# Kernel tuning notes

Hardware: AMD Instinct MI355X
Metric: run time of the kernel (lower is better)

## Reference

```python
import jax, jax.numpy as jnp
import numpy as np


def setup_inputs() -> dict:
    key = jax.random.key(0)
    k1, k2 = jax.random.split(key)
    shape = (16, 3, 512, 512)
    y_true = jax.random.uniform(k1, shape, dtype=jnp.float32)
    y_pred = jax.random.uniform(k2, shape, dtype=jnp.float32)
    return {"y_true": y_true, "y_pred": y_pred}


def reference(y_true, y_pred):
    B, C, W, H = y_true.shape
    percent = 0.4
    index = int(W * H * percent - 1)  # quantile index into ascending sort
    # gray1 = mean over the 3 channels of y_pred  -> [B, W, H]
    gray = (y_pred[:, 0] + y_pred[:, 1] + y_pred[:, 2]) / 3.0
    # torch.topk(-gray, n)[0][:, index] == -(ascending-sorted gray)[index]
    thr = jnp.sort(gray.reshape(B, W * H), axis=1)[:, index]  # [B]
    mask = (gray <= thr[:, None, None]).astype(y_pred.dtype)  # [B, W, H]
    mask = mask[:, None, :, :]  # broadcast over 3 channels
    # mask*|y_pred - y_true| == |mask*y_pred - mask*y_true| since mask in {0,1}
    d = jnp.abs(y_pred - y_true)
    w = mask * 0.8 + (1.0 - mask) * 0.2
    return jnp.mean(w * d)
```

## Files before the change

### kernel.cpp

```cpp
#include <hip/hip_runtime.h>
#include <stdint.h>

#define NB 16
#define NPIX 262144
#define K_RANK 104856u
#define NB1 4096
#define CHUNK_CAP 256
#define CAP 65536
#define SENT 0xFFFFFFFFu
#define PAD(i) ((i) + ((i) >> 4))

__global__ void k_gray_hist(const float* __restrict__ yp, unsigned* __restrict__ hist1,
                            unsigned* __restrict__ zr, int zcount) {
    __shared__ unsigned h[NB1];
    const int tid = threadIdx.x;
    const int gtid = blockIdx.x * 256 + tid;
    if (gtid < zcount) zr[gtid] = 0;
    for (int i = tid; i < NB1; i += 256) h[i] = 0;
    __syncthreads();

    const int blk   = blockIdx.x;
    const int b     = blk >> 8;
    const int chunk = blk & 255;
    const long base = (long)b * 3 * NPIX;
    const int  o    = (chunk * 256 + tid) * 4;

    const float4 c0 = *(const float4*)(yp + base + o);
    const float4 c1 = *(const float4*)(yp + base + NPIX + o);
    const float4 c2 = *(const float4*)(yp + base + 2 * NPIX + o);

    float g0 = (c0.x + c1.x + c2.x) / 3.0f;
    float g1 = (c0.y + c1.y + c2.y) / 3.0f;
    float g2 = (c0.z + c1.z + c2.z) / 3.0f;
    float g3 = (c0.w + c1.w + c2.w) / 3.0f;

    atomicAdd(&h[__float_as_uint(g0) >> 20], 1u);
    atomicAdd(&h[__float_as_uint(g1) >> 20], 1u);
    atomicAdd(&h[__float_as_uint(g2) >> 20], 1u);
    atomicAdd(&h[__float_as_uint(g3) >> 20], 1u);
    __syncthreads();

    unsigned* gh = hist1 + b * NB1;
    for (int i = tid; i < NB1; i += 256) {
        unsigned v = h[i];
        if (v) atomicAdd(&gh[i], v);
    }
}

__global__ void k_scan1(const unsigned* __restrict__ hist1,
                        unsigned* __restrict__ rank1, unsigned* __restrict__ bin1) {
    __shared__ unsigned sh[NB1 + (NB1 >> 4)];
    __shared__ unsigned wave_sums[4];
    const int b   = blockIdx.x;
    const int tid = threadIdx.x;
    const unsigned* hb = hist1 + b * NB1;

    for (int i = tid; i < NB1; i += 256) sh[PAD(i)] = hb[i];
    __syncthreads();

    unsigned sum = 0;
    #pragma unroll
    for (int j = 0; j < 16; ++j) sum += sh[tid * 17 + j];
    unsigned inc = sum;
    for (int off = 1; off < 64; off <<= 1) {
        unsigned v = __shfl_up(inc, off);
        if ((tid & 63) >= off) inc += v;
    }
    if ((tid & 63) == 63) wave_sums[tid >> 6] = inc;
    __syncthreads();
    unsigned woff = 0;
    for (int w = 0; w < (tid >> 6); ++w) woff += wave_sums[w];
    const unsigned excl = woff + inc - sum;

    const unsigned r = K_RANK;
    if (r >= excl && r < excl + sum) {
        unsigned cum = excl;
        unsigned d   = (unsigned)(tid * 16);
        #pragma unroll
        for (int j = 0; j < 16; ++j) {
            unsigned c = sh[tid * 17 + j];
            if (cum + c > r) { d = (unsigned)(tid * 16 + j); break; }
            cum += c;
        }
        rank1[b] = r - cum;
        bin1[b]  = d;
    }
}

__global__ void k_collect(const float* __restrict__ yp, const unsigned* __restrict__ bin1,
                          unsigned* __restrict__ cand, unsigned* __restrict__ hist2) {
    __shared__ unsigned buf[1024];
    __shared__ unsigned cnt;
    const int tid = threadIdx.x;
    if (tid == 0) cnt = 0;
    __syncthreads();

    const int blk   = blockIdx.x;
    const int b     = blk >> 8;
    const int chunk = blk & 255;
    const long base = (long)b * 3 * NPIX;
    const int  o    = (chunk * 256 + tid) * 4;

    const float4 c0 = *(const float4*)(yp + base + o);
    const float4 c1 = *(const float4*)(yp + base + NPIX + o);
    const float4 c2 = *(const float4*)(yp + base + 2 * NPIX + o);

    float g[4];
    g[0] = (c0.x + c1.x + c2.x) / 3.0f;
    g[1] = (c0.y + c1.y + c2.y) / 3.0f;
    g[2] = (c0.z + c1.z + c2.z) / 3.0f;
    g[3] = (c0.w + c1.w + c2.w) / 3.0f;

    const unsigned sel = bin1[b];
    #pragma unroll
    for (int k = 0; k < 4; ++k) {
        unsigned u = __float_as_uint(g[k]);
        if ((u >> 20) == sel) {
            unsigned i = atomicAdd(&cnt, 1u);
            buf[i] = u;
        }
    }
    __syncthreads();
    const unsigned n = (cnt < CHUNK_CAP) ? cnt : CHUNK_CAP;
    unsigned v = SENT;
    if ((unsigned)tid < n) {
        v = buf[tid];
        atomicAdd(&hist2[b * NB1 + ((v >> 8) & 0xFFFu)], 1u);
    }
    cand[(long)b * CAP + chunk * CHUNK_CAP + tid] = v;
}

__global__ void k_selfinal(const unsigned* __restrict__ cand,
                           const unsigned* __restrict__ hist2,
                           const unsigned* __restrict__ rank1, const unsigned* __restrict__ bin1,
                           unsigned* __restrict__ rank2, unsigned* __restrict__ pre2,
                           unsigned* __restrict__ hist3) {
    __shared__ unsigned sh[NB1 + (NB1 >> 4)];
    __shared__ unsigned wave_sums[4];
    __shared__ unsigned s_pre, s_rank;
    const int tid  = threadIdx.x;
    const int b    = blockIdx.x >> 4;
    const int part = blockIdx.x & 15;

    const unsigned* hb = hist2 + b * NB1;
    for (int i = tid; i < NB1; i += 256) sh[PAD(i)] = hb[i];
    __syncthreads();

    unsigned sum = 0;
    #pragma unroll
    for (int j = 0; j < 16; ++j) sum += sh[tid * 17 + j];
    unsigned inc = sum;
    for (int off = 1; off < 64; off <<= 1) {
        unsigned v = __shfl_up(inc, off);
        if ((tid & 63) >= off) inc += v;
    }
    if ((tid & 63) == 63) wave_sums[tid >> 6] = inc;
    __syncthreads();
    unsigned woff = 0;
    for (int w = 0; w < (tid >> 6); ++w) woff += wave_sums[w];
    const unsigned excl = woff + inc - sum;

    const unsigned r = rank1[b];
    if (r >= excl && r < excl + sum) {
        unsigned cum = excl;
        unsigned d   = (unsigned)(tid * 16);
        #pragma unroll
        for (int j = 0; j < 16; ++j) {
            unsigned c = sh[tid * 17 + j];
            if (cum + c > r) { d = (unsigned)(tid * 16 + j); break; }
            cum += c;
        }
        s_rank = r - cum;
        s_pre  = (bin1[b] << 12) | d;
        if (part == 0) { rank2[b] = r - cum; pre2[b] = s_pre; }
    }
    __syncthreads();
    const unsigned pre = s_pre;

    const uint4* cb = (const uint4*)(cand + (long)b * CAP + (long)part * (CAP / 16));
    #pragma unroll
    for (int i = 0; i < 4; ++i) {
        uint4 v = cb[i * 256 + tid];
        if ((v.x >> 8) == pre) atomicAdd(&hist3[b * 256 + (v.x & 0xFFu)], 1u);
        if ((v.y >> 8) == pre) atomicAdd(&hist3[b * 256 + (v.y & 0xFFu)], 1u);
        if ((v.z >> 8) == pre) atomicAdd(&hist3[b * 256 + (v.z & 0xFFu)], 1u);
        if ((v.w >> 8) == pre) atomicAdd(&hist3[b * 256 + (v.w & 0xFFu)], 1u);
    }
}

__global__ void k_loss(const float* __restrict__ yt, const float* __restrict__ yp,
                       const unsigned* __restrict__ hist3,
                       const unsigned* __restrict__ rank2, const unsigned* __restrict__ pre2,
                       double* __restrict__ accum) {
    __shared__ unsigned wave_sums[4];
    __shared__ unsigned bc_thr;
    __shared__ float wsum[4];
    const int tid   = threadIdx.x;
    const int blk   = blockIdx.x;
    const int b     = blk >> 8;
    const int chunk = blk & 255;

    const unsigned sum = hist3[b * 256 + tid];
    unsigned inc = sum;
    for (int off = 1; off < 64; off <<= 1) {
        unsigned v = __shfl_up(inc, off);
        if ((tid & 63) >= off) inc += v;
    }
    if ((tid & 63) == 63) wave_sums[tid >> 6] = inc;
    __syncthreads();
    unsigned woff = 0;
    for (int w = 0; w < (tid >> 6); ++w) woff += wave_sums[w];
    const unsigned excl = woff + inc - sum;
    const unsigned r = rank2[b];
    if (sum > 0 && r >= excl && r < excl + sum) {
        bc_thr = (pre2[b] << 8) | (unsigned)tid;
    }
    __syncthreads();
    const unsigned thr = bc_thr;

    const long base = (long)b * 3 * NPIX;
    const int  o    = (chunk * 256 + tid) * 4;

    float4 p0 = *(const float4*)(yp + base + o);
    float4 p1 = *(const float4*)(yp + base + NPIX + o);
    float4 p2 = *(const float4*)(yp + base + 2 * NPIX + o);
    float4 t0 = *(const float4*)(yt + base + o);
    float4 t1 = *(const float4*)(yt + base + NPIX + o);
    float4 t2 = *(const float4*)(yt + base + 2 * NPIX + o);

    float s = 0.0f;
    {
        float g = (p0.x + p1.x + p2.x) / 3.0f;
        float w = (__float_as_uint(g) <= thr) ? 0.8f : 0.2f;
        s += w * (fabsf(p0.x - t0.x) + fabsf(p1.x - t1.x) + fabsf(p2.x - t2.x));
    }
    {
        float g = (p0.y + p1.y + p2.y) / 3.0f;
        float w = (__float_as_uint(g) <= thr) ? 0.8f : 0.2f;
        s += w * (fabsf(p0.y - t0.y) + fabsf(p1.y - t1.y) + fabsf(p2.y - t2.y));
    }
    {
        float g = (p0.z + p1.z + p2.z) / 3.0f;
        float w = (__float_as_uint(g) <= thr) ? 0.8f : 0.2f;
        s += w * (fabsf(p0.z - t0.z) + fabsf(p1.z - t1.z) + fabsf(p2.z - t2.z));
    }
    {
        float g = (p0.w + p1.w + p2.w) / 3.0f;
        float w = (__float_as_uint(g) <= thr) ? 0.8f : 0.2f;
        s += w * (fabsf(p0.w - t0.w) + fabsf(p1.w - t1.w) + fabsf(p2.w - t2.w));
    }

    for (int off = 32; off > 0; off >>= 1) s += __shfl_down(s, off);
    if ((tid & 63) == 0) wsum[tid >> 6] = s;
    __syncthreads();
    if (tid == 0) {
        float tot = wsum[0] + wsum[1] + wsum[2] + wsum[3];
        atomicAdd(&accum[(blk & 63) * 16], (double)tot);
    }
}

__global__ void k_final(const double* __restrict__ accum, float* __restrict__ out) {
    const int tid = threadIdx.x;
    double v = accum[tid * 16];
    for (int off = 32; off > 0; off >>= 1) v += __shfl_down(v, off);
    if (tid == 0) out[0] = (float)(v / 12582912.0);
}

extern "C" void kernel_launch(void* const* d_in, const int* in_sizes, int n_in,
                              void* d_out, int out_size, void* d_ws, size_t ws_size,
                              hipStream_t stream) {
    const float* yt = (const float*)d_in[0];
    const float* yp = (const float*)d_in[1];
    float* out = (float*)d_out;
    char* ws = (char*)d_ws;

    unsigned* hist1 = (unsigned*)(ws);
    unsigned* zr    = (unsigned*)(ws + 262144);
    unsigned* hist2 = (unsigned*)(ws + 262144);
    unsigned* hist3 = (unsigned*)(ws + 524288);
    double*   accum = (double*)(ws + 540672);
    unsigned* rank1 = (unsigned*)(ws + 548864);
    unsigned* bin1  = (unsigned*)(ws + 548928);
    unsigned* rank2 = (unsigned*)(ws + 548992);
    unsigned* pre2  = (unsigned*)(ws + 549056);
    unsigned* cand  = (unsigned*)(ws + (1 << 20));
    const int zcount = (262144 + 16384 + 8192) / 4;

    hipMemsetAsync(hist1, 0, 262144, stream);

    k_gray_hist<<<4096, 256, 0, stream>>>(yp, hist1, zr, zcount);
    k_scan1<<<NB, 256, 0, stream>>>(hist1, rank1, bin1);
    k_collect<<<4096, 256, 0, stream>>>(yp, bin1, cand, hist2);
    k_selfinal<<<256, 256, 0, stream>>>(cand, hist2, rank1, bin1, rank2, pre2, hist3);
    k_loss<<<4096, 256, 0, stream>>>(yt, yp, hist3, rank2, pre2, accum);
    k_final<<<1, 64, 0, stream>>>(accum, out);
}
```

Measured before the change: 154.1 us.

## Cache gray values, fuse scan into collect, and fold final reduction into loss

After: 328.3 us. 113% more time.

```diff
diff --git a/kernel.cpp b/kernel.cpp
--- a/kernel.cpp
+++ b/kernel.cpp
@@ -11,6 +11,7 @@
 #define PAD(i) ((i) + ((i) >> 4))
 
 __global__ void k_gray_hist(const float* __restrict__ yp, unsigned* __restrict__ hist1,
+                            unsigned* __restrict__ gray,
                             unsigned* __restrict__ zr, int zcount) {
     __shared__ unsigned h[NB1];
     const int tid = threadIdx.x;
@@ -29,15 +30,18 @@
     const float4 c1 = *(const float4*)(yp + base + NPIX + o);
     const float4 c2 = *(const float4*)(yp + base + 2 * NPIX + o);
 
-    float g0 = (c0.x + c1.x + c2.x) / 3.0f;
-    float g1 = (c0.y + c1.y + c2.y) / 3.0f;
-    float g2 = (c0.z + c1.z + c2.z) / 3.0f;
-    float g3 = (c0.w + c1.w + c2.w) / 3.0f;
-
-    atomicAdd(&h[__float_as_uint(g0) >> 20], 1u);
-    atomicAdd(&h[__float_as_uint(g1) >> 20], 1u);
-    atomicAdd(&h[__float_as_uint(g2) >> 20], 1u);
-    atomicAdd(&h[__float_as_uint(g3) >> 20], 1u);
+    uint4 u;
+    u.x = __float_as_uint((c0.x + c1.x + c2.x) / 3.0f);
+    u.y = __float_as_uint((c0.y + c1.y + c2.y) / 3.0f);
+    u.z = __float_as_uint((c0.z + c1.z + c2.z) / 3.0f);
+    u.w = __float_as_uint((c0.w + c1.w + c2.w) / 3.0f);
+
+    *(uint4*)(gray + (long)b * NPIX + o) = u;
+
+    atomicAdd(&h[u.x >> 20], 1u);
+    atomicAdd(&h[u.y >> 20], 1u);
+    atomicAdd(&h[u.z >> 20], 1u);
+    atomicAdd(&h[u.w >> 20], 1u);
     __syncthreads();
 
     unsigned* gh = hist1 + b * NB1;
@@ -47,14 +51,23 @@
     }
 }
 
-__global__ void k_scan1(const unsigned* __restrict__ hist1,
-                        unsigned* __restrict__ rank1, unsigned* __restrict__ bin1) {
+__global__ void k_collect(const unsigned* __restrict__ gray, const unsigned* __restrict__ hist1,
+                          unsigned* __restrict__ rank1, unsigned* __restrict__ bin1,
+                          unsigned* __restrict__ cand, unsigned* __restrict__ hist2) {
     __shared__ unsigned sh[NB1 + (NB1 >> 4)];
     __shared__ unsigned wave_sums[4];
-    const int b   = blockIdx.x;
-    const int tid = threadIdx.x;
+    __shared__ unsigned s_bin, s_rank;
+    __shared__ unsigned buf[1024];
+    __shared__ unsigned cnt;
+    const int tid   = threadIdx.x;
+    const int blk   = blockIdx.x;
+    const int b     = blk >> 8;
+    const int chunk = blk & 255;
+    if (tid == 0) cnt = 0;
+
+    const uint4 g = *(const uint4*)(gray + (long)b * NPIX + (chunk * 256 + tid) * 4);
+
     const unsigned* hb = hist1 + b * NB1;
-
     for (int i = tid; i < NB1; i += 256) sh[PAD(i)] = hb[i];
     __syncthreads();
 
@@ -82,42 +95,19 @@
             if (cum + c > r) { d = (unsigned)(tid * 16 + j); break; }
             cum += c;
         }
-        rank1[b] = r - cum;
-        bin1[b]  = d;
-    }
-}
-
-__global__ void k_collect(const float* __restrict__ yp, const unsigned* __restrict__ bin1,
-                          unsigned* __restrict__ cand, unsigned* __restrict__ hist2) {
-    __shared__ unsigned buf[1024];
-    __shared__ unsigned cnt;
-    const int tid = threadIdx.x;
-    if (tid == 0) cnt = 0;
-    __syncthreads();
-
-    const int blk   = blockIdx.x;
-    const int b     = blk >> 8;
-    const int chunk = blk & 255;
-    const long base = (long)b * 3 * NPIX;
-    const int  o    = (chunk * 256 + tid) * 4;
-
-    const float4 c0 = *(const float4*)(yp + base + o);
-    const float4 c1 = *(const float4*)(yp + base + NPIX + o);
-    const float4 c2 = *(const float4*)(yp + base + 2 * NPIX + o);
-
-    float g[4];
-    g[0] = (c0.x + c1.x + c2.x) / 3.0f;
-    g[1] = (c0.y + c1.y + c2.y) / 3.0f;
-    g[2] = (c0.z + c1.z + c2.z) / 3.0f;
-    g[3] = (c0.w + c1.w + c2.w) / 3.0f;
-
-    const unsigned sel = bin1[b];
+        s_rank = r - cum;
+        s_bin  = d;
+    }
+    __syncthreads();
+    const unsigned sel = s_bin;
+    if (chunk == 0 && tid == 0) { rank1[b] = s_rank; bin1[b] = s_bin; }
+
+    unsigned uu[4] = {g.x, g.y, g.z, g.w};
     #pragma unroll
     for (int k = 0; k < 4; ++k) {
-        unsigned u = __float_as_uint(g[k]);
-        if ((u >> 20) == sel) {
+        if ((uu[k] >> 20) == sel) {
             unsigned i = atomicAdd(&cnt, 1u);
-            buf[i] = u;
+            buf[i] = uu[k];
         }
     }
     __syncthreads();
@@ -191,10 +181,12 @@
 __global__ void k_loss(const float* __restrict__ yt, const float* __restrict__ yp,
                        const unsigned* __restrict__ hist3,
                        const unsigned* __restrict__ rank2, const unsigned* __restrict__ pre2,
-                       double* __restrict__ accum) {
+                       double* __restrict__ accum, unsigned* __restrict__ fincnt,
+                       float* __restrict__ out) {
     __shared__ unsigned wave_sums[4];
     __shared__ unsigned bc_thr;
     __shared__ float wsum[4];
+    __shared__ unsigned s_is_last;
     const int tid   = threadIdx.x;
     const int blk   = blockIdx.x;
     const int b     = blk >> 8;
@@ -256,14 +248,17 @@
     if (tid == 0) {
         float tot = wsum[0] + wsum[1] + wsum[2] + wsum[3];
         atomicAdd(&accum[(blk & 63) * 16], (double)tot);
-    }
-}
-
-__global__ void k_final(const double* __restrict__ accum, float* __restrict__ out) {
-    const int tid = threadIdx.x;
-    double v = accum[tid * 16];
-    for (int off = 32; off > 0; off >>= 1) v += __shfl_down(v, off);
-    if (tid == 0) out[0] = (float)(v / 12582912.0);
+        __threadfence();
+        unsigned done = atomicAdd(fincnt, 1u);
+        s_is_last = (done == 4095u) ? 1u : 0u;
+    }
+    __syncthreads();
+
+    if (s_is_last && tid < 64) {
+        double v = atomicAdd(&accum[tid * 16], 0.0);
+        for (int off = 32; off > 0; off >>= 1) v += __shfl_down(v, off);
+        if (tid == 0) out[0] = (float)(v / 12582912.0);
+    }
 }
 
 extern "C" void kernel_launch(void* const* d_in, const int* in_sizes, int n_in,
@@ -274,24 +269,24 @@
     float* out = (float*)d_out;
     char* ws = (char*)d_ws;
 
-    unsigned* hist1 = (unsigned*)(ws);
-    unsigned* zr    = (unsigned*)(ws + 262144);
-    unsigned* hist2 = (unsigned*)(ws + 262144);
-    unsigned* hist3 = (unsigned*)(ws + 524288);
-    double*   accum = (double*)(ws + 540672);
-    unsigned* rank1 = (unsigned*)(ws + 548864);
-    unsigned* bin1  = (unsigned*)(ws + 548928);
-    unsigned* rank2 = (unsigned*)(ws + 548992);
-    unsigned* pre2  = (unsigned*)(ws + 549056);
-    unsigned* cand  = (unsigned*)(ws + (1 << 20));
-    const int zcount = (262144 + 16384 + 8192) / 4;
+    unsigned* hist1  = (unsigned*)(ws);
+    unsigned* zr     = (unsigned*)(ws + 262144);
+    unsigned* hist2  = (unsigned*)(ws + 262144);
+    unsigned* hist3  = (unsigned*)(ws + 524288);
+    double*   accum  = (double*)(ws + 540672);
+    unsigned* fincnt = (unsigned*)(ws + 548864);
+    unsigned* rank1  = (unsigned*)(ws + 549120);
+    unsigned* bin1   = (unsigned*)(ws + 549184);
+    unsigned* rank2  = (unsigned*)(ws + 549248);
+    unsigned* pre2   = (unsigned*)(ws + 549312);
+    unsigned* cand   = (unsigned*)(ws + (1 << 20));
+    unsigned* gray   = (unsigned*)(ws + (8 << 20));
+    const int zcount = (262144 + 16384 + 8192 + 256) / 4;
 
     hipMemsetAsync(hist1, 0, 262144, stream);
 
-    k_gray_hist<<<4096, 256, 0, stream>>>(yp, hist1, zr, zcount);
-    k_scan1<<<NB, 256, 0, stream>>>(hist1, rank1, bin1);
-    k_collect<<<4096, 256, 0, stream>>>(yp, bin1, cand, hist2);
+    k_gray_hist<<<4096, 256, 0, stream>>>(yp, hist1, gray, zr, zcount);
+    k_collect<<<4096, 256, 0, stream>>>(gray, hist1, rank1, bin1, cand, hist2);
     k_selfinal<<<256, 256, 0, stream>>>(cand, hist2, rank1, bin1, rank2, pre2, hist3);
-    k_loss<<<4096, 256, 0, stream>>>(yt, yp, hist3, rank2, pre2, accum);
-    k_final<<<1, 64, 0, stream>>>(accum, out);
-}
+    k_loss<<<4096, 256, 0, stream>>>(yt, yp, hist3, rank2, pre2, accum, fincnt, out);
+}
```
